# Performance work log

Measured on AMD Instinct MI355X. Metric: run time of the kernel, lower is better.

The kernel has to match this reference:

```python
import jax, jax.numpy as jnp
import numpy as np

H, C, L = 2, 32, 25
EPS = 1e-5


def setup_inputs() -> dict:
    key = jax.random.key(0)
    ks = jax.random.split(key, 12)
    N, E = 20000, 100000
    x_input = jax.random.normal(ks[0], (N, 5), jnp.float32)
    # edges with no self loops (module uses add_self_loops=True, which first removes them)
    src = jax.random.randint(ks[1], (L, E), 0, N, dtype=jnp.int32)
    off = jax.random.randint(ks[2], (L, E), 1, N, dtype=jnp.int32)
    dst = (src + off) % N
    edge_indices = jnp.stack([src, dst], axis=1)              # [L, 2, E]
    edge_weights = jax.random.uniform(ks[3], (L, E, 1), jnp.float32)
    g = lambda k, shp, fan: jax.random.normal(k, shp, jnp.float32) / np.float32(np.sqrt(fan))
    return {
        "x_input": x_input,
        "edge_indices": edge_indices,
        "edge_weights": edge_weights,
        "Wl": g(ks[4], (L, 5, H * C), 5),
        "bl": jnp.zeros((L, H * C), jnp.float32),
        "Wr": g(ks[5], (L, 5, H * C), 5),
        "br": jnp.zeros((L, H * C), jnp.float32),
        "We": g(ks[6], (L, 1, H * C), 1),
        "att": g(ks[7], (L, H, C), C),
        "conv_bias": jnp.zeros((L, C), jnp.float32),
        "gamma1": jnp.ones((L, C), jnp.float32),
        "beta1": jnp.zeros((L, C), jnp.float32),
        "W1": g(ks[8], (800, 800), 800),
        "b1": jnp.zeros((800,), jnp.float32),
        "W2": g(ks[9], (800, 5), 800),
        "b2": jnp.zeros((5,), jnp.float32),
    }


def reference(x_input, edge_indices, edge_weights, Wl, bl, Wr, br, We, att,
              conv_bias, gamma1, beta1, W1, b1, W2, b2):
    N = x_input.shape[0]
    loops = jnp.arange(N, dtype=edge_indices.dtype)

    def layer(carry, p):
        ei, ew, wl, bl_, wr, br_, we, a, cb, g_, be_ = p
        src, dst = ei[0], ei[1]
        ones_e = jnp.ones((src.shape[0],), x_input.dtype)
        # add_self_loops with fill_value='mean': loop attr = mean of incoming edge attrs
        cnt = jax.ops.segment_sum(ones_e, dst, num_segments=N)
        loop_attr = jax.ops.segment_sum(ew, dst, num_segments=N) / jnp.maximum(cnt, 1.0)[:, None]
        s2 = jnp.concatenate([src, loops])
        d2 = jnp.concatenate([dst, loops])
        ea = jnp.concatenate([ew, loop_attr], axis=0)          # [E+N, 1]
        xl = (x_input @ wl + bl_).reshape(N, H, C)             # source transform
        xr = (x_input @ wr + br_).reshape(N, H, C)             # target transform
        eh = jax.nn.leaky_relu(xl[s2] + xr[d2] + (ea @ we).reshape(-1, H, C), 0.2)
        alpha = jnp.einsum('ehc,hc->eh', eh, a)                # [E+N, H]
        amax = jax.ops.segment_max(alpha, d2, num_segments=N)
        alpha = jnp.exp(alpha - amax[d2])
        alpha = alpha / jax.ops.segment_sum(alpha, d2, num_segments=N)[d2]
        msg = (xl[s2] * alpha[:, :, None]).reshape(-1, H * C)
        deg = jax.ops.segment_sum(jnp.ones((s2.shape[0],), x_input.dtype), d2, num_segments=N)
        out = (jax.ops.segment_sum(msg, d2, num_segments=N) / deg[:, None]).reshape(N, H, C)
        out = out.mean(axis=1) + cb                            # concat=False -> mean over heads, + bias
        mu = out.mean(axis=0)
        var = out.var(axis=0)                                  # BatchNorm1d, training-mode batch stats
        out = g_ * (out - mu) * jax.lax.rsqrt(var + EPS) + be_
        return carry, jax.nn.leaky_relu(out, 0.01)

    _, hs = jax.lax.scan(layer, None,
                         (edge_indices, edge_weights, Wl, bl, Wr, br, We, att,
                          conv_bias, gamma1, beta1))            # [L, N, C]
    h = jnp.transpose(hs, (1, 0, 2)).reshape(N, L * C)          # cat along feature dim
    h = jax.nn.relu(h @ W1 + b1)
    return h @ W2 + b2
```

## Files before the change

kernel.cpp:

```cpp
#include <hip/hip_runtime.h>
#include <hip/hip_bf16.h>

#define N_NODES 20000
#define N_EDGES 100000
#define N_LAYERS 25
#define NPAD 20096
#define EPS_BN 1e-5f
#define LOG2E 1.44269504088896340736f
#define NL_NN (N_LAYERS * N_NODES)
#define TOTAL_E (N_LAYERS * N_EDGES)
#define TOTAL_SLOTS (TOTAL_E + NL_NN)
#define SCAN_BLKS ((NL_NN + 1023) / 1024)
#define QUARTER_N 5000
#define CNT_BLKS (N_LAYERS * 4)
#define W1T_END (CNT_BLKS + 700)
#define XPAD_END (W1T_END + 157)
#define HPAD_BLKS 75
#define PREP_BLKS (XPAD_END + HPAD_BLKS)
#define EDGE_BLKS ((TOTAL_E + 1023) / 1024)
#define FILL_BLKS (EDGE_BLKS + SCAN_BLKS)
#define NGRP 14
#define NPW 8
#define NPL (N_NODES / NPW)
#define ATTN_WAVES (NL_NN / NPW)
#define ATTN_BLKS (ATTN_WAVES / 4)
#define G1_BLKS (7 * 157)

typedef short short8 __attribute__((ext_vector_type(8)));
typedef short short4v __attribute__((ext_vector_type(4)));
typedef float floatx4 __attribute__((ext_vector_type(4)));
typedef int int8v __attribute__((ext_vector_type(8)));
typedef int int2v __attribute__((ext_vector_type(2)));
typedef int int4v __attribute__((ext_vector_type(4)));

template <int PAT>
__device__ __forceinline__ float swz(float v) {
  return __int_as_float(__builtin_amdgcn_ds_swizzle(__float_as_int(v), PAT));
}

template <int CTRL>
__device__ __forceinline__ float dpp_add(float v) {
  int r = __builtin_amdgcn_update_dpp(0, __float_as_int(v), CTRL, 0xF, 0xF, true);
  return v + __int_as_float(r);
}

__device__ __forceinline__ float xadd16(float p) {
#if __has_builtin(__builtin_amdgcn_permlane16_swap)
  int2v r = __builtin_amdgcn_permlane16_swap(__float_as_int(p),
                                             __float_as_int(p), false, false);
  return __int_as_float(r[0]) + __int_as_float(r[1]);
#else
  return p + swz<0x401F>(p);
#endif
}

__device__ __forceinline__ float ldbf(const unsigned short* __restrict__ p, int idx) {
  return __uint_as_float((unsigned)p[idx] << 16);
}

__device__ __forceinline__ unsigned short bfbits(float v) {
  return __builtin_bit_cast(unsigned short, (__hip_bfloat16)v);
}

__device__ __forceinline__ void gl_lds16(const short* g, short* l) {
  __builtin_amdgcn_global_load_lds(
      (const __attribute__((address_space(1))) void*)g,
      (__attribute__((address_space(3))) void*)l, 16, 0, 0);
}

__device__ __forceinline__ int8v sload8(const void* p) {
  int8v r;
  asm volatile(
      "s_load_dwordx8 %0, %1, 0x0\n\t"
      "s_waitcnt lgkmcnt(0)"
      : "=s"(r)
      : "s"(p));
  return r;
}

__device__ __forceinline__ void sload_rp(const void* p, int8v& a, int8v& b) {
  asm volatile(
      "s_load_dwordx8 %0, %2, 0x0\n\t"
      "s_load_dwordx8 %1, %2, 0x20\n\t"
      "s_waitcnt lgkmcnt(0)"
      : "=s"(a), "=s"(b)
      : "s"(p));
}

__device__ __forceinline__ void red4(float& p0, float& p1, float& p2, float& p3) {
  asm volatile(
      "s_nop 1\n\t"
      "v_add_f32_dpp %0, %0, %0 quad_perm:[1,0,3,2] row_mask:0xf bank_mask:0xf\n\t"
      "v_add_f32_dpp %1, %1, %1 quad_perm:[1,0,3,2] row_mask:0xf bank_mask:0xf\n\t"
      "v_add_f32_dpp %2, %2, %2 quad_perm:[1,0,3,2] row_mask:0xf bank_mask:0xf\n\t"
      "v_add_f32_dpp %3, %3, %3 quad_perm:[1,0,3,2] row_mask:0xf bank_mask:0xf\n\t"
      "v_add_f32_dpp %0, %0, %0 quad_perm:[2,3,0,1] row_mask:0xf bank_mask:0xf\n\t"
      "v_add_f32_dpp %1, %1, %1 quad_perm:[2,3,0,1] row_mask:0xf bank_mask:0xf\n\t"
      "v_add_f32_dpp %2, %2, %2 quad_perm:[2,3,0,1] row_mask:0xf bank_mask:0xf\n\t"
      "v_add_f32_dpp %3, %3, %3 quad_perm:[2,3,0,1] row_mask:0xf bank_mask:0xf\n\t"
      "v_add_f32_dpp %0, %0, %0 row_half_mirror row_mask:0xf bank_mask:0xf\n\t"
      "v_add_f32_dpp %1, %1, %1 row_half_mirror row_mask:0xf bank_mask:0xf\n\t"
      "v_add_f32_dpp %2, %2, %2 row_half_mirror row_mask:0xf bank_mask:0xf\n\t"
      "v_add_f32_dpp %3, %3, %3 row_half_mirror row_mask:0xf bank_mask:0xf\n\t"
      "v_add_f32_dpp %0, %0, %0 row_mirror row_mask:0xf bank_mask:0xf\n\t"
      "v_add_f32_dpp %1, %1, %1 row_mirror row_mask:0xf bank_mask:0xf\n\t"
      "v_add_f32_dpp %2, %2, %2 row_mirror row_mask:0xf bank_mask:0xf\n\t"
      "v_add_f32_dpp %3, %3, %3 row_mirror row_mask:0xf bank_mask:0xf\n\t"
      "s_nop 1"
      : "+v"(p0), "+v"(p1), "+v"(p2), "+v"(p3));
}

__global__ __launch_bounds__(1024) void prep_kernel(
    const int* __restrict__ ei, const float* __restrict__ ew,
    const float* __restrict__ x, const float* __restrict__ W1,
    int* __restrict__ cnt, int* __restrict__ rank,
    float* __restrict__ wsumg, float* __restrict__ xpad,
    __hip_bfloat16* __restrict__ W1bT, unsigned short* __restrict__ hn) {
  __shared__ int smem[QUARTER_N];
  __shared__ float fsm[QUARTER_N];
  int b = blockIdx.x;
  if (b < CNT_BLKS) {
    int l = b >> 2, base = (b & 3) * QUARTER_N;
    for (int i = threadIdx.x; i < QUARTER_N; i += 1024) {
      smem[i] = 0;
      fsm[i] = 0.f;
    }
    __syncthreads();
    const int* dstp = ei + (size_t)l * 2 * N_EDGES + N_EDGES;
    const float* ewp = ew + (size_t)l * N_EDGES;
    int* rkp = rank + l * N_EDGES;
    for (int e = threadIdx.x; e < N_EDGES; e += 1024) {
      int d = dstp[e] - base;
      if ((unsigned)d < (unsigned)QUARTER_N) {
        rkp[e] = atomicAdd(&smem[d], 1);
        atomicAdd(&fsm[d], ewp[e]);
      }
    }
    __syncthreads();
    int* outp = cnt + l * N_NODES + base;
    float* wp = wsumg + l * N_NODES + base;
    for (int i = threadIdx.x; i < QUARTER_N; i += 1024) {
      outp[i] = smem[i];
      wp[i] = fsm[i];
    }
  } else if (b < W1T_END) {
    float* tile = (float*)smem;
    int bb = b - CNT_BLKS;
    int j0 = (bb % 28) * 32, k0 = (bb / 28) * 32;
    int tx = threadIdx.x & 31, ty = threadIdx.x >> 5;
    tile[ty * 33 + tx] = (j0 + tx < 800) ? W1[(k0 + ty) * 800 + j0 + tx] : 0.f;
    __syncthreads();
    W1bT[(size_t)(j0 + ty) * 800 + k0 + tx] = (__hip_bfloat16)tile[tx * 33 + ty];
  } else if (b < XPAD_END) {
    int idx = (b - W1T_END) * 1024 + threadIdx.x;
    if (idx < N_NODES * 8) {
      int nn = idx >> 3, k = idx & 7;
      xpad[idx] = (k < 5) ? x[nn * 5 + k] : 0.f;
    }
  } else {
    int idx = (b - XPAD_END) * 1024 + threadIdx.x;
    const int per_l = (NPAD - N_NODES) * 32;
    if (idx < N_LAYERS * per_l) {
      int l = idx / per_l;
      int rem = idx - l * per_l;
      hn[((size_t)l * NPAD + N_NODES) * 32 + rem] = 0;
    }
  }
}

__global__ __launch_bounds__(1024) void scan_a(const int* __restrict__ cnt,
                                               int* __restrict__ scn,
                                               int* __restrict__ btot,
                                               float* __restrict__ gsum,
                                               float* __restrict__ gsumsq) {
  int t = threadIdx.x, b = blockIdx.x;
  int i = b * 1024 + t;
  int lane = t & 63, wv = t >> 6;
  int v = (i < NL_NN) ? cnt[i] + 1 : 0;
  int sc = v;
#pragma unroll
  for (int off = 1; off < 64; off <<= 1) {
    int u = __shfl_up(sc, off);
    if (lane >= off) sc += u;
  }
  __shared__ int ws[16];
  if (lane == 63) ws[wv] = sc;
  __syncthreads();
  if (t < 16) {
    int xx = ws[t];
#pragma unroll
    for (int off = 1; off < 16; off <<= 1) {
      int u = __shfl_up(xx, off);
      if (t >= off) xx += u;
    }
    ws[t] = xx;
  }
  __syncthreads();
  int bofs = wv ? ws[wv - 1] : 0;
  if (i < NL_NN) scn[i] = bofs + sc - v;
  if (t == 0) btot[b] = ws[15];
  if (b == 200 && t < N_LAYERS * 32) {
    gsum[t] = 0.f;
    gsumsq[t] = 0.f;
  }
}

__global__ __launch_bounds__(512) void scan_b(const int* __restrict__ btot,
                                              int* __restrict__ boff) {
  int t = threadIdx.x;
  int lane = t & 63, wv = t >> 6;
  int v = (t < SCAN_BLKS) ? btot[t] : 0;
  int sc = v;
#pragma unroll
  for (int off = 1; off < 64; off <<= 1) {
    int u = __shfl_up(sc, off);
    if (lane >= off) sc += u;
  }
  __shared__ int ws[8];
  if (lane == 63) ws[wv] = sc;
  __syncthreads();
  if (t < 8) {
    int xx = ws[t];
#pragma unroll
    for (int off = 1; off < 8; off <<= 1) {
      int u = __shfl_up(xx, off);
      if (t >= off) xx += u;
    }
    ws[t] = xx;
  }
  __syncthreads();
  int bofs = wv ? ws[wv - 1] : 0;
  if (t < SCAN_BLKS) boff[t] = bofs + sc - v;
}

__global__ __launch_bounds__(1024) void fill_kernel(const int* __restrict__ ei,
                                                    const float* __restrict__ ew,
                                                    const int* __restrict__ scn,
                                                    const int* __restrict__ boff,
                                                    const int* __restrict__ rank,
                                                    const float* __restrict__ wsumg,
                                                    const float* __restrict__ xpad,
                                                    int* __restrict__ rowptr,
                                                    int* __restrict__ epr) {
  int b = blockIdx.x;
  if (b < EDGE_BLKS) {
    int idx = b * 1024 + threadIdx.x;
    if (idx >= TOTAL_E) return;
    int l = idx / N_EDGES, e = idx - l * N_EDGES;
    int src = ei[(size_t)l * 2 * N_EDGES + e];
    int dst = ei[(size_t)l * 2 * N_EDGES + N_EDGES + e];
    int g = l * N_NODES + dst;
    int pos = scn[g] + boff[g >> 10] + rank[idx];
    float w = ew[(size_t)l * N_EDGES + e];
    float4 xv = *(const float4*)(xpad + (size_t)src * 8);
    float x4v = xpad[(size_t)src * 8 + 4];
    int4v r;
    r[0] = __float_as_int(w);
    r[1] = (int)bfbits(xv.x) | ((int)bfbits(xv.y) << 16);
    r[2] = (int)bfbits(xv.z) | ((int)bfbits(xv.w) << 16);
    r[3] = (int)bfbits(x4v);
    *(int4v*)(epr + (size_t)pos * 4) = r;
  } else {
    int i = (b - EDGE_BLKS) * 1024 + threadIdx.x;
    if (i < NL_NN) {
      int st = scn[i] + boff[i >> 10];
      int en = (i + 1 < NL_NN) ? scn[i + 1] + boff[(i + 1) >> 10] : TOTAL_SLOTS;
      rowptr[i] = st;
      int cw = en - st - 1;
      float wm = wsumg[i] * __builtin_amdgcn_rcpf(fmaxf((float)cw, 1.f));
      int n = i - (i / N_NODES) * N_NODES;
      float4 xv = *(const float4*)(xpad + (size_t)n * 8);
      float x4v = xpad[(size_t)n * 8 + 4];
      int4v r;
      r[0] = __float_as_int(wm);
      r[1] = (int)bfbits(xv.x) | ((int)bfbits(xv.y) << 16);
      r[2] = (int)bfbits(xv.z) | ((int)bfbits(xv.w) << 16);
      r[3] = (int)bfbits(x4v);
      *(int4v*)(epr + (size_t)(en - 1) * 4) = r;
    }
    if (i < 31) rowptr[NL_NN + i] = TOTAL_SLOTS;
    if (i < 8) {
      int4v z = {0, 0, 0, 0};
      *(int4v*)(epr + (size_t)(TOTAL_SLOTS + i) * 4) = z;
    }
  }
}

__global__ __launch_bounds__(256) void attn_kernel(
    const float* __restrict__ xpad, const int* __restrict__ rowptr,
    const int* __restrict__ epr,
    const float* __restrict__ Wl, const float* __restrict__ bl,
    const float* __restrict__ Wr, const float* __restrict__ br,
    const float* __restrict__ We, const float* __restrict__ att,
    const float* __restrict__ cbias, unsigned short* __restrict__ out_pre,
    float* __restrict__ gsum, float* __restrict__ gsumsq) {
  __shared__ float sb[256];
  int b = blockIdx.x;
  const int q = ATTN_BLKS >> 3, r = ATTN_BLKS & 7;
  int xcd = b & 7, ib = b >> 3;
  int nb = (xcd < r ? xcd * (q + 1) : r * (q + 1) + (xcd - r) * q) + ib;
  int tid = threadIdx.x;
  int w = tid >> 6;
  int wid = __builtin_amdgcn_readfirstlane(nb * 4 + w);
  int lane = tid & 63;
  int l = wid / NPL;
  int n0 = (wid - l * NPL) * NPW;

  float wlv0 = Wl[(l * 5 + 0) * 64 + lane];
  float wlv1 = Wl[(l * 5 + 1) * 64 + lane];
  float wlv2 = Wl[(l * 5 + 2) * 64 + lane];
  float wlv3 = Wl[(l * 5 + 3) * 64 + lane];
  float wlv4 = Wl[(l * 5 + 4) * 64 + lane];
  float wr0 = Wr[(l * 5 + 0) * 64 + lane];
  float wr1 = Wr[(l * 5 + 1) * 64 + lane];
  float wr2 = Wr[(l * 5 + 2) * 64 + lane];
  float wr3 = Wr[(l * 5 + 3) * 64 + lane];
  float wr4 = Wr[(l * 5 + 4) * 64 + lane];
  float blv = bl[l * 64 + lane];
  float brv = br[l * 64 + lane];
  float wev = We[l * 64 + lane];
  float att2v = att[l * 64 + lane] * LOG2E;
  float cbv = cbias[l * 32 + (lane & 31)];

  int8v rpa, rpb;
  sload_rp(rowptr + (size_t)wid * 8, rpa, rpb);

  float s1 = 0.f, s2 = 0.f;

#pragma unroll
  for (int i = 0; i < NPW; i++) {
    int st = rpa[i & 7];
    int en = (i == 7) ? rpb[0] : rpa[(i + 1) & 7];
    int valid = en - st;

    int8v xn = sload8(xpad + (size_t)(n0 + i) * 8);
    float xrn = brv;
    xrn = fmaf(__int_as_float(xn[0]), wr0, xrn);
    xrn = fmaf(__int_as_float(xn[1]), wr1, xrn);
    xrn = fmaf(__int_as_float(xn[2]), wr2, xrn);
    xrn = fmaf(__int_as_float(xn[3]), wr3, xrn);
    xrn = fmaf(__int_as_float(xn[4]), wr4, xrn);

    float ssum = 0.f, acc = 0.f;
    int nchunk = (valid + 3) >> 2;
    for (int c = 0; c < nchunk; c++) {
      int8v r0, r1;
      sload_rp((const char*)epr + (size_t)(st + c * 4) * 16, r0, r1);
      int m = valid - c * 4;
      float xa[4], pk[4];
#define RD(k, j) ((k) < 2 ? r0[(k)*4 + (j)] : r1[((k)-2) * 4 + (j)])
#pragma unroll
      for (int k = 0; k < 4; k++) {
        float wgt = __int_as_float(RD(k, 0));
        int d1 = RD(k, 1), d2 = RD(k, 2), d3 = RD(k, 3);
        float x0 = __int_as_float(d1 << 16);
        float x1 = __int_as_float(d1 & (int)0xffff0000);
        float x2 = __int_as_float(d2 << 16);
        float x3 = __int_as_float(d2 & (int)0xffff0000);
        float x4 = __int_as_float(d3 << 16);
        float a = fmaf(x0, wlv0, blv);
        a = fmaf(x1, wlv1, a);
        a = fmaf(x2, wlv2, a);
        a = fmaf(x3, wlv3, a);
        a = fmaf(x4, wlv4, a);
        xa[k] = a;
        float v = a + fmaf(wgt, wev, xrn);
        float lk = fmaxf(v, 0.2f * v);
        pk[k] = lk * att2v;
      }
#undef RD
      red4(pk[0], pk[1], pk[2], pk[3]);
#pragma unroll
      for (int k = 0; k < 4; k++) pk[k] = xadd16(pk[k]);
#pragma unroll
      for (int k = 0; k < 4; k++) {
        float pe = __builtin_amdgcn_exp2f(pk[k]);
        pe = (k < m) ? pe : 0.f;
        ssum += pe;
        acc = fmaf(xa[k], pe, acc);
      }
    }
    float outv = acc * __builtin_amdgcn_rcpf(ssum * (float)valid);
    float o2 = outv + __shfl_xor(outv, 32);
    float oval = 0.5f * o2 + cbv;
    if (lane < 32)
      out_pre[((size_t)wid * NPW + i) * 32 + lane] = bfbits(oval);
    s1 += oval;
    s2 = fmaf(oval, oval, s2);
  }
  sb[tid] = (lane < 32) ? s1 : s2;
  __syncthreads();
  if (tid < 64) {
    float t = sb[tid] + sb[tid + 64] + sb[tid + 128] + sb[tid + 192];
    if (tid < 32)
      atomicAdd(&gsum[l * 32 + tid], t);
    else
      atomicAdd(&gsumsq[l * 32 + tid - 32], t);
  }
}

__global__ __launch_bounds__(256) void norm_kernel(const unsigned short* __restrict__ out_pre,
                                                   const float* __restrict__ gsum,
                                                   const float* __restrict__ gsumsq,
                                                   const float* __restrict__ gamma,
                                                   const float* __restrict__ beta,
                                                   unsigned short* __restrict__ hn) {
  int idx = blockIdx.x * 256 + threadIdx.x;
  int l = idx / (N_NODES * 8);
  int rem = idx - l * (N_NODES * 8);
  int n = rem >> 3, q = rem & 7;
  int c0 = q * 4;
  short4v v4 = *(const short4v*)(out_pre + (l * N_NODES + n) * 32 + c0);
  short4v o;
#pragma unroll
  for (int i = 0; i < 4; i++) {
    int c = c0 + i;
    float mu = gsum[l * 32 + c] * (1.f / N_NODES);
    float var = gsumsq[l * 32 + c] * (1.f / N_NODES) - mu * mu;
    float vv = __uint_as_float((unsigned)(unsigned short)v4[i] << 16);
    float v = gamma[l * 32 + c] * (vv - mu) * rsqrtf(var + EPS_BN) + beta[l * 32 + c];
    v = v > 0.f ? v : 0.01f * v;
    o[i] = (short)bfbits(v);
  }
  *(short4v*)(hn + ((size_t)l * NPAD + n) * 32 + c0) = o;
}

__global__ __launch_bounds__(256) void gemm1_kernel(const short* __restrict__ hn,
                                                    const short* __restrict__ W1bT,
                                                    const float* __restrict__ b1,
                                                    const float* __restrict__ W2,
                                                    float* __restrict__ p) {
  __shared__ __align__(16) short As[128 * 32];
  __shared__ __align__(16) short Bs[128 * 32];
  const int q = G1_BLKS >> 3, r = G1_BLKS & 7;
  int bf = blockIdx.x;
  int xcd = bf & 7, ib = bf >> 3;
  int nb = (xcd < r ? xcd * (q + 1) : r * (q + 1) + (xcd - r) * q) + ib;
  int mt = nb / 7, nt = nb - mt * 7;
  int n0 = nt * 128, m0 = mt * 128;
  int t = threadIdx.x;
  int wave = t >> 6, lane = t & 63;
  int wr = wave >> 1, wc = wave & 1;
  int mrow = lane & 15, quad = lane >> 4;
  floatx4 acc[4][4];
#pragma unroll
  for (int i = 0; i < 4; i++)
#pragma unroll
    for (int j = 0; j < 4; j++) acc[i][j] = (floatx4){0.f, 0.f, 0.f, 0.f};

  int r0 = t >> 2, s0 = t & 3;
  int r1 = (t + 256) >> 2, s1 = (t + 256) & 3;
  const short* aG0 = hn + (m0 + r0) * 32 + s0 * 8;
  const short* aG1 = hn + (m0 + r1) * 32 + s1 * 8;
  const short* bG0 = W1bT + (n0 + r0) * 800 + s0 * 8;
  const short* bG1 = W1bT + (n0 + r1) * 800 + s1 * 8;
  const int ak = NPAD * 32;
  short* aD0 = As + wave * 512;
  short* aD1 = As + 2048 + wave * 512;
  short* bD0 = Bs + wave * 512;
  short* bD1 = Bs + 2048 + wave * 512;

  for (int kt = 0; kt < 25; kt++) {
    gl_lds16(aG0, aD0);
    gl_lds16(aG1, aD1);
    gl_lds16(bG0, bD0);
    gl_lds16(bG1, bD1);
    aG0 += ak; aG1 += ak; bG0 += 32; bG1 += 32;
    __syncthreads();
    short8 af[4], bfr[4];
#pragma unroll
    for (int i = 0; i < 4; i++)
      af[i] = *(const short8*)(&As[(wr * 64 + i * 16 + mrow) * 32 + quad * 8]);
#pragma unroll
    for (int j = 0; j < 4; j++)
      bfr[j] = *(const short8*)(&Bs[(wc * 64 + j * 16 + mrow) * 32 + quad * 8]);
#pragma unroll
    for (int i = 0; i < 4; i++)
#pragma unroll
      for (int j = 0; j < 4; j++)
        acc[i][j] = __builtin_amdgcn_mfma_f32_16x16x32_bf16(af[i], bfr[j], acc[i][j], 0, 0, 0);
    __syncthreads();
  }

  float w2v[4][5];
  float b1v[4];
#pragma unroll
  for (int j = 0; j < 4; j++) {
    int col = n0 + wc * 64 + j * 16 + mrow;
    bool ok = col < 800;
    b1v[j] = ok ? b1[col] : 0.f;
#pragma unroll
    for (int jj = 0; jj < 5; jj++) w2v[j][jj] = ok ? W2[col * 5 + jj] : 0.f;
  }
  int grp = nt * 2 + wc;
#pragma unroll
  for (int i = 0; i < 4; i++) {
#pragma unroll
    for (int rr = 0; rr < 4; rr++) {
      float s[5] = {0.f, 0.f, 0.f, 0.f, 0.f};
#pragma unroll
      for (int j = 0; j < 4; j++) {
        float v = fmaxf(acc[i][j][rr] + b1v[j], 0.f);
#pragma unroll
        for (int jj = 0; jj < 5; jj++) s[jj] = fmaf(v, w2v[j][jj], s[jj]);
      }
#pragma unroll
      for (int jj = 0; jj < 5; jj++) {
        s[jj] = dpp_add<0xB1>(s[jj]);
        s[jj] = dpp_add<0x4E>(s[jj]);
        s[jj] = dpp_add<0x141>(s[jj]);
        s[jj] = dpp_add<0x140>(s[jj]);
      }
      int row = m0 + wr * 64 + i * 16 + quad * 4 + rr;
      if (mrow == 0) {
#pragma unroll
        for (int jj = 0; jj < 5; jj++)
          p[(row * NGRP + grp) * 5 + jj] = s[jj];
      }
    }
  }
}

__global__ __launch_bounds__(256) void gemm2r_kernel(const float* __restrict__ p,
                                                     const float* __restrict__ b2,
                                                     float* __restrict__ out) {
  int idx = blockIdx.x * 256 + threadIdx.x;
  if (idx >= N_NODES * 5) return;
  int row = idx / 5, jj = idx - row * 5;
  float s = b2[jj];
#pragma unroll
  for (int g = 0; g < NGRP; g++) s += p[(row * NGRP + g) * 5 + jj];
  out[idx] = s;
}

extern "C" void kernel_launch(void* const* d_in, const int* in_sizes, int n_in,
                              void* d_out, int out_size, void* d_ws, size_t ws_size,
                              hipStream_t stream) {
  const float* x    = (const float*)d_in[0];
  const int*   ei   = (const int*)d_in[1];
  const float* ew   = (const float*)d_in[2];
  const float* Wl   = (const float*)d_in[3];
  const float* bl   = (const float*)d_in[4];
  const float* Wr   = (const float*)d_in[5];
  const float* br   = (const float*)d_in[6];
  const float* We   = (const float*)d_in[7];
  const float* att  = (const float*)d_in[8];
  const float* cb   = (const float*)d_in[9];
  const float* gam  = (const float*)d_in[10];
  const float* bet  = (const float*)d_in[11];
  const float* W1   = (const float*)d_in[12];
  const float* b1   = (const float*)d_in[13];
  const float* W2   = (const float*)d_in[14];
  const float* b2   = (const float*)d_in[15];

  char* ws = (char*)d_ws;
  size_t off = 0;
  auto alloc = [&](size_t bytes) {
    void* p = ws + off;
    off = (off + bytes + 255) & ~(size_t)255;
    return p;
  };
  int* cnt     = (int*)alloc((size_t)NL_NN * 4);
  int* scn     = (int*)alloc((size_t)NL_NN * 4);
  int* btot    = (int*)alloc(SCAN_BLKS * 4);
  int* boff    = (int*)alloc(SCAN_BLKS * 4);
  int* rank    = (int*)alloc((size_t)TOTAL_E * 4);
  int* rowptr  = (int*)alloc((size_t)(NL_NN + 32) * 4);
  float* wsumg = (float*)alloc((size_t)NL_NN * 4);
  int* epr     = (int*)alloc((size_t)TOTAL_SLOTS * 16 + 256);
  unsigned short* out_pre = (unsigned short*)alloc((size_t)NL_NN * 32 * 2);
  float* gsum   = (float*)alloc(N_LAYERS * 32 * 4);
  float* gsumsq = (float*)alloc(N_LAYERS * 32 * 4);
  float* xpad   = (float*)alloc((size_t)N_NODES * 8 * 4);
  __hip_bfloat16* w1t = (__hip_bfloat16*)alloc((size_t)896 * 800 * 2);
  float* pbuf = (float*)alloc((size_t)NPAD * NGRP * 5 * 4);
  unsigned short* hn = (unsigned short*)alloc((size_t)N_LAYERS * NPAD * 32 * 2);

  prep_kernel<<<PREP_BLKS, 1024, 0, stream>>>(ei, ew, x, W1, cnt, rank, wsumg,
                                              xpad, w1t, hn);
  scan_a<<<SCAN_BLKS, 1024, 0, stream>>>(cnt, scn, btot, gsum, gsumsq);
  scan_b<<<1, 512, 0, stream>>>(btot, boff);
  fill_kernel<<<FILL_BLKS, 1024, 0, stream>>>(ei, ew, scn, boff, rank, wsumg,
                                              xpad, rowptr, epr);
  attn_kernel<<<ATTN_BLKS, 256, 0, stream>>>(
      xpad, rowptr, epr, Wl, bl, Wr, br, We, att, cb, out_pre, gsum, gsumsq);
  norm_kernel<<<(NL_NN * 8) / 256, 256, 0, stream>>>(
      out_pre, gsum, gsumsq, gam, bet, hn);
  gemm1_kernel<<<G1_BLKS, 256, 0, stream>>>(
      (const short*)hn, (const short*)w1t, b1, W2, pbuf);
  gemm2r_kernel<<<(N_NODES * 5 + 255) / 256, 256, 0, stream>>>(
      pbuf, b2, (float*)d_out);
}
```

Measured before the change: 444.9 us.

## Fuse batchnorm and leaky-relu into GEMM A-tile load, drop norm kernel

Removes the separate normalisation pass that wrote a padded bf16 activation buffer. A tiny kernel now precomputes a per-channel scale and shift, and the GEMM applies scale, shift and leaky-relu while loading its A tile from the raw pre-norm output. Out-of-range rows are zero-filled, so the padding writes are dropped. This saves a full read and write of the activations and one launch. In exchange, the A loads go through registers instead of direct-to-LDS copies, and the normalisation is recomputed for each column tile.

```diff
diff --git a/kernel.cpp b/kernel.cpp
--- a/kernel.cpp
+++ b/kernel.cpp
@@ -4,7 +4,6 @@
 #define N_NODES 20000
 #define N_EDGES 100000
 #define N_LAYERS 25
-#define NPAD 20096
 #define EPS_BN 1e-5f
 #define LOG2E 1.44269504088896340736f
 #define NL_NN (N_LAYERS * N_NODES)
@@ -15,8 +14,7 @@
 #define CNT_BLKS (N_LAYERS * 4)
 #define W1T_END (CNT_BLKS + 700)
 #define XPAD_END (W1T_END + 157)
-#define HPAD_BLKS 75
-#define PREP_BLKS (XPAD_END + HPAD_BLKS)
+#define PREP_BLKS XPAD_END
 #define EDGE_BLKS ((TOTAL_E + 1023) / 1024)
 #define FILL_BLKS (EDGE_BLKS + SCAN_BLKS)
 #define NGRP 14
@@ -115,7 +113,7 @@
     const float* __restrict__ x, const float* __restrict__ W1,
     int* __restrict__ cnt, int* __restrict__ rank,
     float* __restrict__ wsumg, float* __restrict__ xpad,
-    __hip_bfloat16* __restrict__ W1bT, unsigned short* __restrict__ hn) {
+    __hip_bfloat16* __restrict__ W1bT) {
   __shared__ int smem[QUARTER_N];
   __shared__ float fsm[QUARTER_N];
   int b = blockIdx.x;
@@ -151,19 +149,11 @@
     tile[ty * 33 + tx] = (j0 + tx < 800) ? W1[(k0 + ty) * 800 + j0 + tx] : 0.f;
     __syncthreads();
     W1bT[(size_t)(j0 + ty) * 800 + k0 + tx] = (__hip_bfloat16)tile[tx * 33 + ty];
-  } else if (b < XPAD_END) {
+  } else {
     int idx = (b - W1T_END) * 1024 + threadIdx.x;
     if (idx < N_NODES * 8) {
       int nn = idx >> 3, k = idx & 7;
       xpad[idx] = (k < 5) ? x[nn * 5 + k] : 0.f;
-    }
-  } else {
-    int idx = (b - XPAD_END) * 1024 + threadIdx.x;
-    const int per_l = (NPAD - N_NODES) * 32;
-    if (idx < N_LAYERS * per_l) {
-      int l = idx / per_l;
-      int rem = idx - l * per_l;
-      hn[((size_t)l * NPAD + N_NODES) * 32 + rem] = 0;
     }
   }
 }
@@ -399,37 +389,25 @@
   }
 }
 
-__global__ __launch_bounds__(256) void norm_kernel(const unsigned short* __restrict__ out_pre,
-                                                   const float* __restrict__ gsum,
-                                                   const float* __restrict__ gsumsq,
-                                                   const float* __restrict__ gamma,
-                                                   const float* __restrict__ beta,
-                                                   unsigned short* __restrict__ hn) {
-  int idx = blockIdx.x * 256 + threadIdx.x;
-  int l = idx / (N_NODES * 8);
-  int rem = idx - l * (N_NODES * 8);
-  int n = rem >> 3, q = rem & 7;
-  int c0 = q * 4;
-  short4v v4 = *(const short4v*)(out_pre + (l * N_NODES + n) * 32 + c0);
-  short4v o;
-#pragma unroll
-  for (int i = 0; i < 4; i++) {
-    int c = c0 + i;
-    float mu = gsum[l * 32 + c] * (1.f / N_NODES);
-    float var = gsumsq[l * 32 + c] * (1.f / N_NODES) - mu * mu;
-    float vv = __uint_as_float((unsigned)(unsigned short)v4[i] << 16);
-    float v = gamma[l * 32 + c] * (vv - mu) * rsqrtf(var + EPS_BN) + beta[l * 32 + c];
-    v = v > 0.f ? v : 0.01f * v;
-    o[i] = (short)bfbits(v);
-  }
-  *(short4v*)(hn + ((size_t)l * NPAD + n) * 32 + c0) = o;
-}
-
-__global__ __launch_bounds__(256) void gemm1_kernel(const short* __restrict__ hn,
-                                                    const short* __restrict__ W1bT,
-                                                    const float* __restrict__ b1,
-                                                    const float* __restrict__ W2,
-                                                    float* __restrict__ p) {
+__global__ __launch_bounds__(1024) void bnparam_kernel(
+    const float* __restrict__ gsum, const float* __restrict__ gsumsq,
+    const float* __restrict__ gamma, const float* __restrict__ beta,
+    float* __restrict__ scA, float* __restrict__ shB) {
+  int idx = threadIdx.x;
+  if (idx < N_LAYERS * 32) {
+    float mu = gsum[idx] * (1.f / N_NODES);
+    float var = gsumsq[idx] * (1.f / N_NODES) - mu * mu;
+    float sc = gamma[idx] * rsqrtf(var + EPS_BN);
+    scA[idx] = sc;
+    shB[idx] = beta[idx] - mu * sc;
+  }
+}
+
+__global__ __launch_bounds__(256) void gemm1_kernel(
+    const unsigned short* __restrict__ out_pre, const short* __restrict__ W1bT,
+    const float* __restrict__ scA, const float* __restrict__ shB,
+    const float* __restrict__ b1, const float* __restrict__ W2,
+    float* __restrict__ p) {
   __shared__ __align__(16) short As[128 * 32];
   __shared__ __align__(16) short Bs[128 * 32];
   const int q = G1_BLKS >> 3, r = G1_BLKS & 7;
@@ -450,22 +428,51 @@
 
   int r0 = t >> 2, s0 = t & 3;
   int r1 = (t + 256) >> 2, s1 = (t + 256) & 3;
-  const short* aG0 = hn + (m0 + r0) * 32 + s0 * 8;
-  const short* aG1 = hn + (m0 + r1) * 32 + s1 * 8;
   const short* bG0 = W1bT + (n0 + r0) * 800 + s0 * 8;
   const short* bG1 = W1bT + (n0 + r1) * 800 + s1 * 8;
-  const int ak = NPAD * 32;
-  short* aD0 = As + wave * 512;
-  short* aD1 = As + 2048 + wave * 512;
   short* bD0 = Bs + wave * 512;
   short* bD1 = Bs + 2048 + wave * 512;
+  int nA0 = m0 + r0, nA1 = m0 + r1;
+  short* aD0 = As + r0 * 32 + s0 * 8;
+  short* aD1 = As + r1 * 32 + s1 * 8;
 
   for (int kt = 0; kt < 25; kt++) {
-    gl_lds16(aG0, aD0);
-    gl_lds16(aG1, aD1);
     gl_lds16(bG0, bD0);
     gl_lds16(bG1, bD1);
-    aG0 += ak; aG1 += ak; bG0 += 32; bG1 += 32;
+    bG0 += 32;
+    bG1 += 32;
+    {
+      short8 av = {0, 0, 0, 0, 0, 0, 0, 0};
+      if (nA0 < N_NODES) {
+        short8 raw = *(const short8*)(out_pre +
+                                      ((size_t)kt * N_NODES + nA0) * 32 + s0 * 8);
+        const float* scp = scA + kt * 32 + s0 * 8;
+        const float* shp = shB + kt * 32 + s0 * 8;
+#pragma unroll
+        for (int j = 0; j < 8; j++) {
+          float v = __uint_as_float((unsigned)(unsigned short)raw[j] << 16);
+          float o = fmaf(v, scp[j], shp[j]);
+          o = o > 0.f ? o : 0.01f * o;
+          av[j] = (short)bfbits(o);
+        }
+      }
+      *(short8*)aD0 = av;
+      short8 av2 = {0, 0, 0, 0, 0, 0, 0, 0};
+      if (nA1 < N_NODES) {
+        short8 raw = *(const short8*)(out_pre +
+                                      ((size_t)kt * N_NODES + nA1) * 32 + s1 * 8);
+        const float* scp = scA + kt * 32 + s1 * 8;
+        const float* shp = shB + kt * 32 + s1 * 8;
+#pragma unroll
+        for (int j = 0; j < 8; j++) {
+          float v = __uint_as_float((unsigned)(unsigned short)raw[j] << 16);
+          float o = fmaf(v, scp[j], shp[j]);
+          o = o > 0.f ? o : 0.01f * o;
+          av2[j] = (short)bfbits(o);
+        }
+      }
+      *(short8*)aD1 = av2;
+    }
     __syncthreads();
     short8 af[4], bfr[4];
 #pragma unroll
@@ -571,23 +578,23 @@
   unsigned short* out_pre = (unsigned short*)alloc((size_t)NL_NN * 32 * 2);
   float* gsum   = (float*)alloc(N_LAYERS * 32 * 4);
   float* gsumsq = (float*)alloc(N_LAYERS * 32 * 4);
+  float* scA    = (float*)alloc(N_LAYERS * 32 * 4);
+  float* shB    = (float*)alloc(N_LAYERS * 32 * 4);
   float* xpad   = (float*)alloc((size_t)N_NODES * 8 * 4);
   __hip_bfloat16* w1t = (__hip_bfloat16*)alloc((size_t)896 * 800 * 2);
-  float* pbuf = (float*)alloc((size_t)NPAD * NGRP * 5 * 4);
-  unsigned short* hn = (unsigned short*)alloc((size_t)N_LAYERS * NPAD * 32 * 2);
+  float* pbuf = (float*)alloc((size_t)20096 * NGRP * 5 * 4);
 
   prep_kernel<<<PREP_BLKS, 1024, 0, stream>>>(ei, ew, x, W1, cnt, rank, wsumg,
-                                              xpad, w1t, hn);
+                                              xpad, w1t);
   scan_a<<<SCAN_BLKS, 1024, 0, stream>>>(cnt, scn, btot, gsum, gsumsq);
   scan_b<<<1, 512, 0, stream>>>(btot, boff);
   fill_kernel<<<FILL_BLKS, 1024, 0, stream>>>(ei, ew, scn, boff, rank, wsumg,
                                               xpad, rowptr, epr);
   attn_kernel<<<ATTN_BLKS, 256, 0, stream>>>(
       xpad, rowptr, epr, Wl, bl, Wr, br, We, att, cb, out_pre, gsum, gsumsq);
-  norm_kernel<<<(NL_NN * 8) / 256, 256, 0, stream>>>(
-      out_pre, gsum, gsumsq, gam, bet, hn);
+  bnparam_kernel<<<1, 1024, 0, stream>>>(gsum, gsumsq, gam, bet, scA, shB);
   gemm1_kernel<<<G1_BLKS, 256, 0, stream>>>(
-      (const short*)hn, (const short*)w1t, b1, W2, pbuf);
+      out_pre, (const short*)w1t, scA, shB, b1, W2, pbuf);
   gemm2r_kernel<<<(N_NODES * 5 + 255) / 256, 256, 0, stream>>>(
       pbuf, b2, (float*)d_out);
 }
```

Result: slower. 455.6 us (+2.4%).
